# Optimization experiments

Hardware: AMD Instinct MI355X
Metric: run time of the kernel (lower is better)

## Reference

```python
import jax, jax.numpy as jnp
import numpy as np

EPS = float(np.finfo(np.float32).eps)  # matches torch.finfo(float32).eps
N_PTS, K_DIM, N_BINS = 1_000_000, 3, 21  # wv_tilde last dim = 2*N_BINS+1 = 43


def setup_inputs() -> dict:
    key = jax.random.key(0)
    k1, k2 = jax.random.split(key)
    # y in the open unit interval (points on the unit hypercube, per-coordinate)
    y = jax.random.uniform(k1, (N_PTS, K_DIM), jnp.float32, 1e-4, 1.0 - 1e-4)
    # network-predicted unnormalized widths/heights: [N, k, 2b+1]
    wv_tilde = jax.random.normal(k2, (N_PTS, K_DIM, 2 * N_BINS + 1), jnp.float32)
    return {"y": y, "wv_tilde": wv_tilde}


def _gather(t, idx):
    # gather along last axis with [..., 1] int index -> [...]
    return jnp.take_along_axis(t, idx, axis=-1)[..., 0]


def pwquad_flow(y, wv_tilde):
    """Faithful JAX port of ElementWisePWQuadraticTransform.flow (with jacobian)."""
    D = wv_tilde.shape[-1]
    nv = (D + 1) // 2                      # ceil(D/2) = b+1 vertex heights
    v_tilde = wv_tilde[..., :nv]           # [N,k,b+1]
    w_tilde = wv_tilde[..., nv:]           # [N,k,b]
    b = w_tilde.shape[-1]

    # normalized bin widths and their cumulative sums
    w = jnp.exp(w_tilde)
    wsum = jnp.cumsum(w, axis=-1)
    wnorm = wsum[..., -1:]
    w = w / wnorm
    wsum = wsum / wnorm
    zeros = jnp.zeros(wsum.shape[:-1] + (1,), wsum.dtype)
    wsum_shift = jnp.concatenate([zeros, wsum], axis=-1)   # [N,k,b+1]

    # modified softmax for vertex heights of the derivative (integrates to 1)
    ve = jnp.exp(v_tilde)
    trap = (ve[..., :-1] + ve[..., 1:]) * 0.5 * w          # trapezoid areas
    v = jnp.maximum(ve / trap.sum(-1, keepdims=True), 1e-6)  # [N,k,b+1]

    # cumulative CDF values at bin edges
    vw = jnp.concatenate(
        [zeros, jnp.cumsum((v[..., :-1] + v[..., 1:]) * 0.5 * w, axis=-1)],
        axis=-1)                                           # [N,k,b+1]

    # argmax-based bin search (identical to torch implementation)
    finder = jnp.where(vw > y[..., None], 0.0, 1.0)
    cat = jnp.concatenate([jnp.full_like(zeros, EPS), finder * (vw + 1.0)], axis=-1)
    mx = jnp.argmax(cat, axis=-1) - 1
    edges = jnp.clip(mx, 0, b - 1).astype(jnp.int32)[..., None]  # [N,k,1]

    v0 = _gather(v, edges)
    v1 = _gather(v, edges + 1)
    we = _gather(w, edges)

    # quadratic solve: (a/2) t^2 + bq t + c = 0  within the bin
    a = (v1 - v0) * we
    bq = v0 * we
    c = _gather(vw, edges) - y
    a = jnp.where(jnp.abs(a) < EPS, EPS, a)
    d = jnp.maximum(bq * bq - 2.0 * a * c, 0.0)
    sq = jnp.sqrt(d)
    sol1 = (-bq - sq) / a
    sol2 = (-bq + sq) / a
    sol = jnp.where((sol1 >= 0.0) & (sol1 < 1.0), sol1, sol2)
    sol = jnp.clip(sol, EPS, 1.0 - EPS)

    x = we * sol + _gather(wsum_shift, edges)
    x = jnp.clip(x, EPS, 1.0 - EPS)

    # log|det J| = -sum log(lerp(v0, v1, sol))
    logj = -jnp.sum(jnp.log(v0 + (v1 - v0) * sol), axis=-1, keepdims=True)
    return x, logj


def reference(y, wv_tilde):
    return pwquad_flow(y, wv_tilde)
```

## Files before the change

### kernel.cpp

```cpp
#include <hip/hip_runtime.h>
#include <math.h>

#define NROWS        3000000
#define NTHREADS     64
#define ROWS_PER_BLK 60
#define NBINS        21
#define NV           22
#define DROW         43
#define F_PER_BLK    (ROWS_PER_BLK * DROW)
#define F4_PER_BLK   (F_PER_BLK / 4)
#define NBLOCKS      (NROWS / ROWS_PER_BLK)

#define AS1 __attribute__((address_space(1)))
#define AS3 __attribute__((address_space(3)))

__device__ __forceinline__ void gload16(const void* g, void* l) {
    __builtin_amdgcn_global_load_lds((const AS1 void*)g, (AS3 void*)l, 16, 0, 0);
}

__global__ __launch_bounds__(NTHREADS, 4) void pwquad_kernel(
    const float* __restrict__ y,
    const float* __restrict__ wv,
    float* __restrict__ out)
{
    __shared__ float buf[F_PER_BLK];
    __shared__ float yb[ROWS_PER_BLK];

    const int tid = threadIdx.x;
    const int b   = blockIdx.x;
    const float EPSF = 1.1920929e-07f;

    {
        const float4* s = reinterpret_cast<const float4*>(wv + (size_t)b * F_PER_BLK);
        float4* d = reinterpret_cast<float4*>(buf);
#pragma unroll
        for (int it = 0; it < 10; ++it)
            gload16(s + it * NTHREADS + tid, d + it * NTHREADS + tid);
        if (tid < (F4_PER_BLK - 10 * NTHREADS))
            gload16(s + 10 * NTHREADS + tid, d + 10 * NTHREADS + tid);
        if (tid < (ROWS_PER_BLK / 4))
            gload16(reinterpret_cast<const float4*>(y + (size_t)b * ROWS_PER_BLK) + tid,
                    reinterpret_cast<float4*>(yb) + tid);
    }
    asm volatile("s_waitcnt vmcnt(0)" ::: "memory");

    float ltv = 0.f;
    if (tid < ROWS_PER_BLK) {
        const float yv = yb[tid];
        const float* myrow = &buf[tid * DROW];

        float w[NBINS];
        float wnorm = 0.f;
#pragma unroll
        for (int j = 0; j < NBINS; ++j) { w[j] = __expf(myrow[NV + j]); wnorm += w[j]; }
        const float invw = 1.0f / wnorm;
#pragma unroll
        for (int j = 0; j < NBINS; ++j) w[j] *= invw;

        float v[NV];
#pragma unroll
        for (int i = 0; i < NV; ++i) v[i] = __expf(myrow[i]);
        float T = 0.f;
#pragma unroll
        for (int j = 0; j < NBINS; ++j) T += (v[j] + v[j + 1]) * 0.5f * w[j];
        const float invT = 1.0f / T;
#pragma unroll
        for (int i = 0; i < NV; ++i) v[i] = fmaxf(v[i] * invT, 1e-6f);

        float vw = 0.f, wsum = 0.f;
        float vwe = 0.f, wse = 0.f;
        float v0 = v[0], v1 = v[1], we = w[0];
#pragma unroll
        for (int j = 0; j < 20; ++j) {
            const float inc = (v[j] + v[j + 1]) * 0.5f * w[j];
            vw += inc;
            wsum += w[j];
            const bool q = (vw <= yv);
            vwe = q ? vw       : vwe;
            wse = q ? wsum     : wse;
            v0  = q ? v[j + 1] : v0;
            v1  = q ? v[j + 2] : v1;
            we  = q ? w[j + 1] : we;
        }

        float a = (v1 - v0) * we;
        const float bq = v0 * we;
        const float cc = vwe - yv;
        a = (fabsf(a) < EPSF) ? EPSF : a;
        const float dd = fmaxf(bq * bq - 2.0f * a * cc, 0.f);
        const float sq = sqrtf(dd);
        const float sol1 = (-bq - sq) / a;
        const float sol2 = (-bq + sq) / a;
        float sol = (sol1 >= 0.f && sol1 < 1.f) ? sol1 : sol2;
        sol = fminf(fmaxf(sol, EPSF), 1.f - EPSF);
        float x = we * sol + wse;
        x = fminf(fmaxf(x, EPSF), 1.f - EPSF);

        out[(size_t)b * ROWS_PER_BLK + tid] = x;
        ltv = __logf(v0 + (v1 - v0) * sol);
    }

    const float t1 = __shfl(ltv, (tid + 1) & 63);
    const float t2 = __shfl(ltv, (tid + 2) & 63);
    if (tid < ROWS_PER_BLK && (tid % 3) == 0) {
        out[NROWS + (size_t)b * (ROWS_PER_BLK / 3) + tid / 3] = -(ltv + t1 + t2);
    }
}

extern "C" void kernel_launch(void* const* d_in, const int* in_sizes, int n_in,
                              void* d_out, int out_size, void* d_ws, size_t ws_size,
                              hipStream_t stream) {
    const float* y  = (const float*)d_in[0];
    const float* wv = (const float*)d_in[1];
    float* out = (float*)d_out;

    pwquad_kernel<<<NBLOCKS, NTHREADS, 0, stream>>>(y, wv, out);
}
```

Before: 105.1 us.

## Convert to persistent grid with double-buffered LDS prefetch of row chunks

The kernel becomes persistent, launching 7 blocks per CU. Each block loops over 60-row chunks and issues the async global-to-LDS load of the next chunk before computing the current one, aiming to overlap memory transfer with the exp/scan math. The y value is now read directly from global memory instead of staged through LDS. The risk: the y load is issued after the prefetch, and in-order vmcnt accounting makes waiting for it also wait for the prefetch, which can cancel the overlap. Far fewer waves per CU also lowers the memory-latency hiding that the oversubscribed grid provided.

```diff
diff --git a/kernel.cpp b/kernel.cpp
--- a/kernel.cpp
+++ b/kernel.cpp
@@ -1,15 +1,16 @@
 #include <hip/hip_runtime.h>
 #include <math.h>
 
-#define NROWS        3000000
-#define NTHREADS     64
-#define ROWS_PER_BLK 60
-#define NBINS        21
-#define NV           22
-#define DROW         43
-#define F_PER_BLK    (ROWS_PER_BLK * DROW)
-#define F4_PER_BLK   (F_PER_BLK / 4)
-#define NBLOCKS      (NROWS / ROWS_PER_BLK)
+#define NROWS   3000000
+#define RPC     60
+#define NCHUNKS (NROWS / RPC)
+#define BPCU    7
+#define GRID    (256 * BPCU)
+#define NBINS   21
+#define NV      22
+#define DROW    43
+#define FPC     (RPC * DROW)
+#define F4PC    (FPC / 4)
 
 #define AS1 __attribute__((address_space(1)))
 #define AS3 __attribute__((address_space(3)))
@@ -18,92 +19,104 @@
     __builtin_amdgcn_global_load_lds((const AS1 void*)g, (AS3 void*)l, 16, 0, 0);
 }
 
-__global__ __launch_bounds__(NTHREADS, 4) void pwquad_kernel(
+__device__ __forceinline__ void prefetch(const float4* __restrict__ wv4,
+                                         int c, float* buf, int tid)
+{
+    const float4* s = wv4 + (size_t)c * F4PC;
+    float4* d = reinterpret_cast<float4*>(buf);
+#pragma unroll
+    for (int it = 0; it < 10; ++it)
+        gload16(s + it * 64 + tid, d + it * 64 + tid);
+    if (tid < (F4PC - 640))
+        gload16(s + 640 + tid, d + 640 + tid);
+}
+
+__global__ __launch_bounds__(64) void pwquad_kernel(
     const float* __restrict__ y,
     const float* __restrict__ wv,
     float* __restrict__ out)
 {
-    __shared__ float buf[F_PER_BLK];
-    __shared__ float yb[ROWS_PER_BLK];
+    __shared__ float buf[2][FPC];
 
     const int tid = threadIdx.x;
-    const int b   = blockIdx.x;
+    const float4* wv4 = reinterpret_cast<const float4*>(wv);
     const float EPSF = 1.1920929e-07f;
 
-    {
-        const float4* s = reinterpret_cast<const float4*>(wv + (size_t)b * F_PER_BLK);
-        float4* d = reinterpret_cast<float4*>(buf);
-#pragma unroll
-        for (int it = 0; it < 10; ++it)
-            gload16(s + it * NTHREADS + tid, d + it * NTHREADS + tid);
-        if (tid < (F4_PER_BLK - 10 * NTHREADS))
-            gload16(s + 10 * NTHREADS + tid, d + 10 * NTHREADS + tid);
-        if (tid < (ROWS_PER_BLK / 4))
-            gload16(reinterpret_cast<const float4*>(y + (size_t)b * ROWS_PER_BLK) + tid,
-                    reinterpret_cast<float4*>(yb) + tid);
-    }
+    prefetch(wv4, blockIdx.x, buf[0], tid);
     asm volatile("s_waitcnt vmcnt(0)" ::: "memory");
 
-    float ltv = 0.f;
-    if (tid < ROWS_PER_BLK) {
-        const float yv = yb[tid];
-        const float* myrow = &buf[tid * DROW];
+    int cur = 0;
+    for (int c = blockIdx.x; c < NCHUNKS; c += GRID) {
+        const int cn = c + GRID;
+        if (cn < NCHUNKS)
+            prefetch(wv4, cn, buf[cur ^ 1], tid);
 
-        float w[NBINS];
-        float wnorm = 0.f;
+        float ltv = 0.f;
+        if (tid < RPC) {
+            const float yv = y[(size_t)c * RPC + tid];
+            const float* myrow = &buf[cur][tid * DROW];
+
+            float w[NBINS];
+            float wnorm = 0.f;
 #pragma unroll
-        for (int j = 0; j < NBINS; ++j) { w[j] = __expf(myrow[NV + j]); wnorm += w[j]; }
-        const float invw = 1.0f / wnorm;
+            for (int j = 0; j < NBINS; ++j) { w[j] = __expf(myrow[NV + j]); wnorm += w[j]; }
+            const float invw = 1.0f / wnorm;
 #pragma unroll
-        for (int j = 0; j < NBINS; ++j) w[j] *= invw;
+            for (int j = 0; j < NBINS; ++j) w[j] *= invw;
 
-        float v[NV];
+            float v[NV];
 #pragma unroll
-        for (int i = 0; i < NV; ++i) v[i] = __expf(myrow[i]);
-        float T = 0.f;
+            for (int i = 0; i < NV; ++i) v[i] = __expf(myrow[i]);
+            float T = 0.f;
 #pragma unroll
-        for (int j = 0; j < NBINS; ++j) T += (v[j] + v[j + 1]) * 0.5f * w[j];
-        const float invT = 1.0f / T;
+            for (int j = 0; j < NBINS; ++j) T += (v[j] + v[j + 1]) * 0.5f * w[j];
+            const float invT = 1.0f / T;
 #pragma unroll
-        for (int i = 0; i < NV; ++i) v[i] = fmaxf(v[i] * invT, 1e-6f);
+            for (int i = 0; i < NV; ++i) v[i] = fmaxf(v[i] * invT, 1e-6f);
 
-        float vw = 0.f, wsum = 0.f;
-        float vwe = 0.f, wse = 0.f;
-        float v0 = v[0], v1 = v[1], we = w[0];
+            float vw = 0.f, wsum = 0.f;
+            float vwe = 0.f, wse = 0.f;
+            float v0 = v[0], v1 = v[1], we = w[0];
 #pragma unroll
-        for (int j = 0; j < 20; ++j) {
-            const float inc = (v[j] + v[j + 1]) * 0.5f * w[j];
-            vw += inc;
-            wsum += w[j];
-            const bool q = (vw <= yv);
-            vwe = q ? vw       : vwe;
-            wse = q ? wsum     : wse;
-            v0  = q ? v[j + 1] : v0;
-            v1  = q ? v[j + 2] : v1;
-            we  = q ? w[j + 1] : we;
+            for (int j = 0; j < 20; ++j) {
+                const float inc = (v[j] + v[j + 1]) * 0.5f * w[j];
+                vw += inc;
+                wsum += w[j];
+                const bool q = (vw <= yv);
+                vwe = q ? vw       : vwe;
+                wse = q ? wsum     : wse;
+                v0  = q ? v[j + 1] : v0;
+                v1  = q ? v[j + 2] : v1;
+                we  = q ? w[j + 1] : we;
+            }
+
+            float a = (v1 - v0) * we;
+            const float bq = v0 * we;
+            const float cc = vwe - yv;
+            a = (fabsf(a) < EPSF) ? EPSF : a;
+            const float dd = fmaxf(bq * bq - 2.0f * a * cc, 0.f);
+            const float sq = sqrtf(dd);
+            const float sol1 = (-bq - sq) / a;
+            const float sol2 = (-bq + sq) / a;
+            float sol = (sol1 >= 0.f && sol1 < 1.f) ? sol1 : sol2;
+            sol = fminf(fmaxf(sol, EPSF), 1.f - EPSF);
+            float x = we * sol + wse;
+            x = fminf(fmaxf(x, EPSF), 1.f - EPSF);
+
+            out[(size_t)c * RPC + tid] = x;
+            ltv = __logf(v0 + (v1 - v0) * sol);
         }
 
-        float a = (v1 - v0) * we;
-        const float bq = v0 * we;
-        const float cc = vwe - yv;
-        a = (fabsf(a) < EPSF) ? EPSF : a;
-        const float dd = fmaxf(bq * bq - 2.0f * a * cc, 0.f);
-        const float sq = sqrtf(dd);
-        const float sol1 = (-bq - sq) / a;
-        const float sol2 = (-bq + sq) / a;
-        float sol = (sol1 >= 0.f && sol1 < 1.f) ? sol1 : sol2;
-        sol = fminf(fmaxf(sol, EPSF), 1.f - EPSF);
-        float x = we * sol + wse;
-        x = fminf(fmaxf(x, EPSF), 1.f - EPSF);
+        const float t1 = __shfl(ltv, (tid + 1) & 63);
+        const float t2 = __shfl(ltv, (tid + 2) & 63);
+        if (tid < RPC && (tid % 3) == 0) {
+            out[NROWS + (size_t)c * (RPC / 3) + tid / 3] = -(ltv + t1 + t2);
+        }
 
-        out[(size_t)b * ROWS_PER_BLK + tid] = x;
-        ltv = __logf(v0 + (v1 - v0) * sol);
-    }
+        if (cn < NCHUNKS)
+            asm volatile("s_waitcnt vmcnt(2)" ::: "memory");
 
-    const float t1 = __shfl(ltv, (tid + 1) & 63);
-    const float t2 = __shfl(ltv, (tid + 2) & 63);
-    if (tid < ROWS_PER_BLK && (tid % 3) == 0) {
-        out[NROWS + (size_t)b * (ROWS_PER_BLK / 3) + tid / 3] = -(ltv + t1 + t2);
+        cur ^= 1;
     }
 }
 
@@ -114,5 +127,5 @@
     const float* wv = (const float*)d_in[1];
     float* out = (float*)d_out;
 
-    pwquad_kernel<<<NBLOCKS, NTHREADS, 0, stream>>>(y, wv, out);
+    pwquad_kernel<<<GRID, 64, 0, stream>>>(y, wv, out);
 }
```

Measured after the change: 111.7 us. +6.4%, slower.
